# Kernel tuning notes

Hardware: AMD Instinct MI355X
Metric: run time of the kernel (lower is better)

## Reference

```python
import jax, jax.numpy as jnp
import numpy as np

NU, NI = 100000, 50000          # sampled users / items in the block
E = 1600000                      # edges (user-item interactions)
D = 64                           # hidden_dims
R = 6                            # num_ratings + 1


def setup_inputs() -> dict:
    key = jax.random.key(0)
    ks = jax.random.split(key, 24)
    f = jax.random.normal
    inp = {
        'user_ids': jax.random.randint(ks[0], (NU,), 0, 500000),
        'item_ids': jax.random.randint(ks[1], (NI,), 0, 200000),
        'gender': jax.random.randint(ks[2], (NU,), 0, 3),
        'genres': jax.random.randint(ks[3], (NI,), 0, 20),
        'edge_user': jax.random.randint(ks[4], (E,), 0, NU),
        'edge_item': jax.random.randint(ks[5], (E,), 0, NI),
        'rating': jax.random.randint(ks[6], (E,), 0, R),
        'user_emb': f(ks[7], (500000, D), jnp.float32),
        'item_emb': f(ks[8], (200000, D), jnp.float32),
        'gender_emb': f(ks[9], (3, D), jnp.float32),
        'genre_emb': f(ks[10], (20, D), jnp.float32),
        'Wr_watched': f(ks[11], (R, D, D), jnp.float32) * 0.1,
        'Wr_watchedby': f(ks[12], (R, D, D), jnp.float32) * 0.1,
        'Ww': f(ks[13], (D, 2 * D), jnp.float32) * 0.1,
        'bw': f(ks[14], (D,), jnp.float32) * 0.1,
        'Wwb': f(ks[15], (D, 2 * D), jnp.float32) * 0.1,
        'bwb': f(ks[16], (D,), jnp.float32) * 0.1,
        'Wf': f(ks[17], (D, D), jnp.float32) * 0.1,
        'bf': f(ks[18], (D,), jnp.float32) * 0.1,
        'Vf': f(ks[19], (D, D), jnp.float32) * 0.1,
        'bv': f(ks[20], (D,), jnp.float32) * 0.1,
    }
    return inp


def _gcmc_conv(Wr, Wlin, blin, h_src, h_dst, src_idx, dst_idx, rating, n_dst):
    # per-node relation transform: [R, N_src, D] (grouped GEMM instead of per-edge [E,D,D])
    X = jnp.einsum('nj,rij->rni', h_src, Wr)
    m = X[rating, src_idx]                              # per-edge message [E, D]
    s = jax.ops.segment_sum(m, dst_idx, num_segments=n_dst)
    cnt = jax.ops.segment_sum(jnp.ones((m.shape[0], 1), m.dtype), dst_idx,
                              num_segments=n_dst)
    h_neigh = s / jnp.maximum(cnt, 1.0)                 # mean; 0 for isolated nodes
    return jax.nn.relu(jnp.concatenate([h_dst, h_neigh], axis=1) @ Wlin.T + blin)


def reference(user_ids, item_ids, gender, genres, edge_user, edge_item, rating,
              user_emb, item_emb, gender_emb, genre_emb,
              Wr_watched, Wr_watchedby, Ww, bw, Wwb, bwb, Wf, bf, Vf, bv):
    hu = user_emb[user_ids] + gender_emb[gender]        # [NU, D]
    hi = item_emb[item_ids] + genre_emb[genres]         # [NI, D]
    # GCMCLayer: 'watched' (user -> item) and 'watchedby' (item -> user)
    hi_new = _gcmc_conv(Wr_watched, Ww, bw, hu, hi, edge_user, edge_item,
                        rating, hi.shape[0])
    hu_new = _gcmc_conv(Wr_watchedby, Wwb, bwb, hi, hu, edge_item, edge_user,
                        rating, hu.shape[0])
    user_out = hu_new @ Wf.T + bf
    item_out = hi_new @ Vf.T + bv
    return user_out, item_out
```

## Files before the change

kernel.cpp:

```cpp
#include <hip/hip_runtime.h>
#include <hip/hip_bf16.h>

#define D 64
#define NRAT 6

typedef float f32x4 __attribute__((ext_vector_type(4)));
typedef short bf16x8 __attribute__((ext_vector_type(8)));

union FragU { uint32_t u[4]; bf16x8 v; };

__device__ __forceinline__ short f2bf(float f) {
    __hip_bfloat16 h = __float2bfloat16(f);
    union { __hip_bfloat16 h; short s; } c; c.h = h; return c.s;
}
__device__ __forceinline__ uint32_t pk2(float a, float b) {
    union { short s[2]; uint32_t u; } c; c.s[0] = f2bf(a); c.s[1] = f2bf(b); return c.u;
}

__global__ void build_h(const int* __restrict__ uid, const int* __restrict__ iid,
                        const int* __restrict__ gender, const int* __restrict__ genres,
                        const float* __restrict__ user_emb, const float* __restrict__ item_emb,
                        const float* __restrict__ gender_emb, const float* __restrict__ genre_emb,
                        unsigned short* __restrict__ hu, unsigned short* __restrict__ hi,
                        int* __restrict__ cntZero, int NU, int NI) {
    int t = blockIdx.x * blockDim.x + threadIdx.x;
    if (t < 512) cntZero[t] = 0;
    int total = (NU + NI) * 16;
    if (t >= total) return;
    int row = t >> 4, c = t & 15;
    uint2 o;
    if (row < NU) {
        int u = uid[row], g = gender[row];
        float4 a = ((const float4*)user_emb)[(size_t)u * 16 + c];
        float4 b = ((const float4*)gender_emb)[(size_t)g * 16 + c];
        o.x = pk2(a.x + b.x, a.y + b.y); o.y = pk2(a.z + b.z, a.w + b.w);
        ((uint2*)hu)[(size_t)row * 16 + c] = o;
    } else {
        int r2 = row - NU;
        int it = iid[r2], ge = genres[r2];
        float4 a = ((const float4*)item_emb)[(size_t)it * 16 + c];
        float4 b = ((const float4*)genre_emb)[(size_t)ge * 16 + c];
        o.x = pk2(a.x + b.x, a.y + b.y); o.y = pk2(a.z + b.z, a.w + b.w);
        ((uint2*)hi)[(size_t)r2 * 16 + c] = o;
    }
}

__global__ __launch_bounds__(256) void hist_both(const int* __restrict__ edge_item,
                                                 const int* __restrict__ edge_user,
                                                 int* __restrict__ cntI, int* __restrict__ cntU,
                                                 int E) {
    __shared__ int hI[256], hU[256];
    hI[threadIdx.x] = 0; hU[threadIdx.x] = 0;
    __syncthreads();
    for (int i = blockIdx.x * blockDim.x + threadIdx.x; i < E; i += gridDim.x * blockDim.x) {
        atomicAdd(&hI[edge_item[i] >> 8], 1);
        atomicAdd(&hU[edge_user[i] >> 9], 1);
    }
    __syncthreads();
    int vi = hI[threadIdx.x], vu = hU[threadIdx.x];
    if (vi) atomicAdd(&cntI[threadIdx.x], vi);
    if (vu) atomicAdd(&cntU[threadIdx.x], vu);
}

__global__ __launch_bounds__(256) void scan_both(const int* __restrict__ cntI,
                                                 const int* __restrict__ cntU,
                                                 int* __restrict__ offI, int* __restrict__ offU,
                                                 int* __restrict__ curI, int* __restrict__ curU,
                                                 int NBI, int NBU, int E) {
    const int* cnt = blockIdx.x ? cntU : cntI;
    int* coarseOff  = blockIdx.x ? offU : offI;
    int* coarseCur  = blockIdx.x ? curU : curI;
    int NB          = blockIdx.x ? NBU : NBI;
    __shared__ int p[256];
    int tid = threadIdx.x;
    int v = (tid < NB) ? cnt[tid] : 0;
    p[tid] = v; __syncthreads();
    for (int dd = 1; dd < 256; dd <<= 1) {
        int a = (tid >= dd) ? p[tid - dd] : 0;
        __syncthreads();
        p[tid] += a;
        __syncthreads();
    }
    int excl = p[tid] - v;
    if (tid < NB) { coarseOff[tid] = excl; coarseCur[tid] = excl; }
    if (tid == 0) coarseOff[NB] = E;
}

__global__ __launch_bounds__(256) void multisplit_A2(
        const int* __restrict__ edge_item, const int* __restrict__ edge_user,
        const int* __restrict__ rating,
        int* __restrict__ curI, int* __restrict__ curU,
        unsigned* __restrict__ staged1, unsigned* __restrict__ staged2,
        int E, int nTiles, int NU, int NI) {
    const bool dirU = blockIdx.x >= nTiles;
    const int* dst = dirU ? edge_user : edge_item;
    const int* src = dirU ? edge_item : edge_user;
    const int shift = dirU ? 9 : 8;
    const int Ns = dirU ? NI : NU;
    int* coarseCur = dirU ? curU : curI;
    unsigned* staged = dirU ? staged2 : staged1;
    const int tile = (dirU ? blockIdx.x - nTiles : blockIdx.x) * 2048;

    __shared__ unsigned srt[2048];
    __shared__ int sft[2048];
    __shared__ int hist[256], pfx[256], shm[256];
    const int tid = threadIdx.x;
    int cnt = E - tile; if (cnt > 2048) cnt = 2048;
    hist[tid] = 0;
    __syncthreads();
    unsigned rec[8]; int bk[8];
    #pragma unroll
    for (int k = 0; k < 8; ++k) {
        int i = tile + k * 256 + tid;
        bk[k] = -1;
        if (i < E) {
            int d = dst[i], s = src[i], r = rating[i];
            bk[k] = d >> shift;
            rec[k] = (unsigned)(s + r * Ns) | ((unsigned)(d & ((1 << shift) - 1)) << 20);
            atomicAdd(&hist[bk[k]], 1);
        }
    }
    __syncthreads();
    pfx[tid] = hist[tid];
    __syncthreads();
    for (int dd = 1; dd < 256; dd <<= 1) {
        int a = (tid >= dd) ? pfx[tid - dd] : 0;
        __syncthreads();
        pfx[tid] += a;
        __syncthreads();
    }
    int h = hist[tid];
    int excl = pfx[tid] - h;
    int gb = 0;
    if (h > 0) gb = atomicAdd(&coarseCur[tid], h);
    shm[tid] = gb - excl;
    __syncthreads();
    hist[tid] = excl;
    __syncthreads();
    #pragma unroll
    for (int k = 0; k < 8; ++k) {
        if (bk[k] >= 0) {
            int p = atomicAdd(&hist[bk[k]], 1);
            srt[p] = rec[k];
            sft[p] = shm[bk[k]];
        }
    }
    __syncthreads();
    for (int i = tid; i < cnt; i += 256)
        staged[sft[i] + i] = srt[i];
}

__global__ __launch_bounds__(256) void multisplit_B2(
        unsigned* __restrict__ staged1, unsigned* __restrict__ staged2,
        const int* __restrict__ coarseOffI, const int* __restrict__ coarseOffU,
        int* __restrict__ offI, int* __restrict__ offU,
        int NBI, int NU, int NI, int E) {
    const bool dirU = (int)blockIdx.x >= NBI;
    unsigned* staged = dirU ? staged2 : staged1;
    const int* coarseOff = dirU ? coarseOffU : coarseOffI;
    int* off = dirU ? offU : offI;
    const int N = dirU ? NU : NI;
    const int shift = dirU ? 9 : 8;
    const int b = dirU ? blockIdx.x - NBI : blockIdx.x;
    const int nb = dirU ? (N + (1 << 9) - 1) >> 9 : NBI;

    __shared__ unsigned rec[16384];
    __shared__ int hist[512], pfx[512];
    const int tid = threadIdx.x;
    const int range = 1 << shift;
    int cbase = coarseOff[b];
    int cnt = coarseOff[b + 1] - cbase;
    if (cnt > 16384) cnt = 16384;
    hist[tid] = 0; hist[tid + 256] = 0;
    __syncthreads();
    for (int i = tid; i < cnt; i += 256) {
        unsigned x = staged[cbase + i];
        rec[i] = x;
        atomicAdd(&hist[x >> 20], 1);
    }
    __syncthreads();
    pfx[tid] = hist[tid]; pfx[tid + 256] = hist[tid + 256];
    __syncthreads();
    for (int dd = 1; dd < 256; dd <<= 1) {
        int a = (tid >= dd) ? pfx[tid - dd] : 0;
        int c = (tid >= dd) ? pfx[tid + 256 - dd] : 0;
        __syncthreads();
        pfx[tid] += a; pfx[tid + 256] += c;
        __syncthreads();
    }
    int tot0 = pfx[255];
    __syncthreads();
    pfx[tid + 256] += tot0;
    __syncthreads();
    int e0 = pfx[tid] - hist[tid];
    int e1 = pfx[tid + 256] - hist[tid + 256];
    __syncthreads();
    hist[tid] = e0; hist[tid + 256] = e1;
    int dbase = b << shift;
    if (dbase + tid < N) off[dbase + tid] = cbase + e0;
    if (range > 256 && dbase + tid + 256 < N) off[dbase + tid + 256] = cbase + e1;
    if (b == nb - 1 && tid == 0) off[N] = E;
    __syncthreads();
    for (int i = tid; i < cnt; i += 256) {
        unsigned x = rec[i];
        int p = atomicAdd(&hist[x >> 20], 1);
        staged[cbase + p] = x;
    }
}

__global__ void prep_weights(const float* __restrict__ Wr_w, const float* __restrict__ Wr_wb,
                             const float* __restrict__ Ww, const float* __restrict__ Wwb,
                             const float* __restrict__ Vf, const float* __restrict__ Wf,
                             short* __restrict__ pWrW, short* __restrict__ pWrWB,
                             short* __restrict__ pWw, short* __restrict__ pWwb,
                             short* __restrict__ pVf, short* __restrict__ pWf) {
    int t = blockIdx.x * blockDim.x + threadIdx.x;
    const float* src; short* dst; int K; int idx;
    if      (t < 24576) { src = Wr_w;  dst = pWrW;  K = 64;  idx = t; }
    else if (t < 49152) { src = Wr_wb; dst = pWrWB; K = 64;  idx = t - 24576; }
    else if (t < 57344) { src = Ww;    dst = pWw;   K = 128; idx = t - 49152; }
    else if (t < 65536) { src = Wwb;   dst = pWwb;  K = 128; idx = t - 57344; }
    else if (t < 69632) { src = Vf;    dst = pVf;   K = 64;  idx = t - 65536; }
    else if (t < 73728) { src = Wf;    dst = pWf;   K = 64;  idx = t - 69632; }
    else return;
    int per  = 64 * K;
    int sub  = idx / per;
    int li   = idx % per;
    int e    = li & 7;
    int lane = (li >> 3) & 63;
    int frag = li >> 9;
    int nkt  = K >> 5;
    int t16  = frag / nkt, tk = frag % nkt;
    int row  = t16 * 16 + (lane & 15);
    int col  = tk * 32 + (lane >> 4) * 8 + e;
    dst[idx] = f2bf(src[((size_t)(sub * 64 + row)) * K + col]);
}

__global__ __launch_bounds__(256) void pretransform2(
        const unsigned short* __restrict__ hu, const unsigned short* __restrict__ hi,
        const short* __restrict__ pWrW, const short* __restrict__ pWrWB,
        unsigned short* __restrict__ y1, unsigned short* __restrict__ y2,
        int NU, int NI, int wavesU) {
    const int lane = threadIdx.x & 63;
    const int m = lane & 15, q = lane >> 4;
    int wave = (blockIdx.x * blockDim.x + threadIdx.x) >> 6;
    const bool dirI = wave >= wavesU;
    const unsigned short* h = dirI ? hi : hu;
    const short* pWr = dirI ? pWrWB : pWrW;
    unsigned short* y = dirI ? y2 : y1;
    const int Ns = dirI ? NI : NU;
    if (dirI) wave -= wavesU;
    const int n0 = wave * 16;
    if (n0 >= Ns) return;
    int nrow = n0 + m; if (nrow > Ns - 1) nrow = Ns - 1;

    bf16x8 bB[2];
    {
        const unsigned short* ph = h + (size_t)nrow * D + q * 8;
        bB[0] = *(const bf16x8*)(ph);
        bB[1] = *(const bf16x8*)(ph + 32);
    }
    const int srcA = ((q & 1) << 5) + m;
    const int srcB = srcA + 16;
    const bool hiq = (q >> 1) != 0;

    #pragma unroll
    for (int r = 0; r < NRAT; ++r) {
        f32x4 acc[4] = {};
        #pragma unroll
        for (int it = 0; it < 4; ++it)
            #pragma unroll
            for (int kt = 0; kt < 2; ++kt) {
                bf16x8 a = *(const bf16x8*)(pWr + (((r * 4 + it) * 2 + kt) << 9) + (lane << 3));
                acc[it] = __builtin_amdgcn_mfma_f32_16x16x32_bf16(a, bB[kt], acc[it], 0, 0, 0);
            }
        uint32_t u0[4], u1[4];
        #pragma unroll
        for (int it = 0; it < 4; ++it) {
            u0[it] = pk2(acc[it][0], acc[it][1]);
            u1[it] = pk2(acc[it][2], acc[it][3]);
        }
        #pragma unroll
        for (int w = 0; w < 2; ++w) {
            uint32_t aa0 = (uint32_t)__shfl((int)u0[2*w],   srcA), bb0 = (uint32_t)__shfl((int)u0[2*w+1], srcA);
            uint32_t aa1 = (uint32_t)__shfl((int)u1[2*w],   srcA), bb1 = (uint32_t)__shfl((int)u1[2*w+1], srcA);
            uint32_t aa2 = (uint32_t)__shfl((int)u0[2*w],   srcB), bb2 = (uint32_t)__shfl((int)u0[2*w+1], srcB);
            uint32_t aa3 = (uint32_t)__shfl((int)u1[2*w],   srcB), bb3 = (uint32_t)__shfl((int)u1[2*w+1], srcB);
            FragU f;
            f.u[0] = hiq ? bb0 : aa0;
            f.u[1] = hiq ? bb1 : aa1;
            f.u[2] = hiq ? bb2 : aa2;
            f.u[3] = hiq ? bb3 : aa3;
            *(bf16x8*)(y + ((size_t)r * Ns + nrow) * D + w * 32 + q * 8) = f.v;
        }
    }
}

__global__ __launch_bounds__(256) void gather_both(
        const int* __restrict__ offI, const int* __restrict__ offU,
        const unsigned* __restrict__ staged1, const unsigned* __restrict__ staged2,
        const unsigned short* __restrict__ y1, const unsigned short* __restrict__ y2,
        unsigned short* __restrict__ hn1, unsigned short* __restrict__ hn2,
        int NI, int NU) {
    int lane = threadIdx.x & 63;
    int g = (blockIdx.x * blockDim.x + threadIdx.x) >> 6;
    const bool dirU = g >= NI;
    int n = dirU ? g - NI : g;
    if (dirU && n >= NU) return;
    const int* off = dirU ? offU : offI;
    const unsigned* packed = dirU ? staged2 : staged1;
    const unsigned short* y = dirU ? y2 : y1;
    unsigned short* hn = dirU ? hn2 : hn1;

    int b = off[n], e = off[n + 1];
    float a0 = 0.f, a1 = 0.f, a2 = 0.f, a3 = 0.f;

#define YLD(mm) __uint_as_float(((unsigned)y[((size_t)((mm) & 0xFFFFFu)) * D + lane]) << 16)

    for (int base = b; base < e; base += 64) {
        int idx = base + lane; if (idx > e - 1) idx = e - 1;
        unsigned meta = packed[idx];
        int cnt = e - base; if (cnt > 64) cnt = 64;
        int j = 0;
        for (; j + 4 <= cnt; j += 4) {
            unsigned m0 = (unsigned)__builtin_amdgcn_readlane((int)meta, j);
            unsigned m1 = (unsigned)__builtin_amdgcn_readlane((int)meta, j + 1);
            unsigned m2 = (unsigned)__builtin_amdgcn_readlane((int)meta, j + 2);
            unsigned m3 = (unsigned)__builtin_amdgcn_readlane((int)meta, j + 3);
            a0 += YLD(m0); a1 += YLD(m1); a2 += YLD(m2); a3 += YLD(m3);
        }
        for (; j < cnt; ++j) {
            unsigned mm = (unsigned)__builtin_amdgcn_readlane((int)meta, j);
            a0 += YLD(mm);
        }
    }
#undef YLD
    float inv = 1.0f / fmaxf((float)(e - b), 1.0f);
    hn[(size_t)n * D + lane] = (unsigned short)f2bf(((a0 + a1) + (a2 + a3)) * inv);
}

__global__ __launch_bounds__(256) void transform_both(
        const unsigned short* __restrict__ hn1, const unsigned short* __restrict__ hn2,
        const unsigned short* __restrict__ hi, const unsigned short* __restrict__ hu,
        const short* __restrict__ pWw, const short* __restrict__ pWwb,
        const float* __restrict__ bw, const float* __restrict__ bwb,
        const short* __restrict__ pVf, const short* __restrict__ pWf,
        const float* __restrict__ bv, const float* __restrict__ bf,
        float* __restrict__ item_out, float* __restrict__ user_out,
        int NI, int NU, int tilesI) {
    const int lane = threadIdx.x & 63;
    const int m = lane & 15, q = lane >> 4;
    int wave = (blockIdx.x * blockDim.x + threadIdx.x) >> 6;
    const bool dirU = wave >= tilesI;
    if (dirU) wave -= tilesI;
    const unsigned short* hn = dirU ? hn2 : hn1;
    const unsigned short* hd = dirU ? hu : hi;
    const short* pWlin = dirU ? pWwb : pWw;
    const float* blin  = dirU ? bwb : bw;
    const short* pW2   = dirU ? pWf : pVf;
    const float* b2    = dirU ? bf : bv;
    float* out = dirU ? user_out : item_out;
    const int N = dirU ? NU : NI;
    const int n0 = wave * 16;
    if (n0 >= N) return;
    int nrow = n0 + m; if (nrow > N - 1) nrow = N - 1;

    bf16x8 bH[2], bHN[2];
    {
        const unsigned short* ph = hd + (size_t)nrow * D + q * 8;
        bH[0] = *(const bf16x8*)(ph);
        bH[1] = *(const bf16x8*)(ph + 32);
        const unsigned short* pn = hn + (size_t)nrow * D + q * 8;
        bHN[0] = *(const bf16x8*)(pn);
        bHN[1] = *(const bf16x8*)(pn + 32);
    }

    f32x4 acc2[4] = {};
    #pragma unroll
    for (int it = 0; it < 4; ++it)
        #pragma unroll
        for (int kt = 0; kt < 4; ++kt) {
            bf16x8 a = *(const bf16x8*)(pWlin + (((it * 4) + kt) << 9) + (lane << 3));
            bf16x8 b = (kt < 2) ? bH[kt] : bHN[kt - 2];
            acc2[it] = __builtin_amdgcn_mfma_f32_16x16x32_bf16(a, b, acc2[it], 0, 0, 0);
        }

    const int srcA = ((q & 1) << 5) + m;
    const int srcB = srcA + 16;
    const bool hiq = (q >> 1) != 0;
    uint32_t u0[4], u1[4];
    float vbl = blin[lane];
    #pragma unroll
    for (int it = 0; it < 4; ++it) {
        float h0 = fmaxf(acc2[it][0] + __shfl(vbl, it * 16 + q * 4 + 0), 0.f);
        float h1 = fmaxf(acc2[it][1] + __shfl(vbl, it * 16 + q * 4 + 1), 0.f);
        float h2 = fmaxf(acc2[it][2] + __shfl(vbl, it * 16 + q * 4 + 2), 0.f);
        float h3 = fmaxf(acc2[it][3] + __shfl(vbl, it * 16 + q * 4 + 3), 0.f);
        u0[it] = pk2(h0, h1);
        u1[it] = pk2(h2, h3);
    }
    bf16x8 bA3[2];
    #pragma unroll
    for (int w = 0; w < 2; ++w) {
        uint32_t aa0 = (uint32_t)__shfl((int)u0[2*w],   srcA), bb0 = (uint32_t)__shfl((int)u0[2*w+1], srcA);
        uint32_t aa1 = (uint32_t)__shfl((int)u1[2*w],   srcA), bb1 = (uint32_t)__shfl((int)u1[2*w+1], srcA);
        uint32_t aa2 = (uint32_t)__shfl((int)u0[2*w],   srcB), bb2 = (uint32_t)__shfl((int)u0[2*w+1], srcB);
        uint32_t aa3 = (uint32_t)__shfl((int)u1[2*w],   srcB), bb3 = (uint32_t)__shfl((int)u1[2*w+1], srcB);
        FragU f;
        f.u[0] = hiq ? bb0 : aa0;
        f.u[1] = hiq ? bb1 : aa1;
        f.u[2] = hiq ? bb2 : aa2;
        f.u[3] = hiq ? bb3 : aa3;
        bA3[w] = f.v;
    }

    f32x4 acc3[4] = {};
    #pragma unroll
    for (int ct = 0; ct < 4; ++ct)
        #pragma unroll
        for (int kt = 0; kt < 2; ++kt) {
            bf16x8 b = *(const bf16x8*)(pW2 + (((ct * 2) + kt) << 9) + (lane << 3));
            acc3[ct] = __builtin_amdgcn_mfma_f32_16x16x32_bf16(bA3[kt], b, acc3[ct], 0, 0, 0);
        }
    #pragma unroll
    for (int ct = 0; ct < 4; ++ct) {
        float bb = b2[ct * 16 + m];
        #pragma unroll
        for (int rg = 0; rg < 4; ++rg) {
            int n = n0 + q * 4 + rg;
            if (n < N) out[(size_t)n * D + ct * 16 + m] = acc3[ct][rg] + bb;
        }
    }
}

extern "C" void kernel_launch(void* const* d_in, const int* in_sizes, int n_in,
                              void* d_out, int out_size, void* d_ws, size_t ws_size,
                              hipStream_t stream) {
    const int*   user_ids   = (const int*)  d_in[0];
    const int*   item_ids   = (const int*)  d_in[1];
    const int*   gender     = (const int*)  d_in[2];
    const int*   genres     = (const int*)  d_in[3];
    const int*   edge_user  = (const int*)  d_in[4];
    const int*   edge_item  = (const int*)  d_in[5];
    const int*   rating     = (const int*)  d_in[6];
    const float* user_emb   = (const float*)d_in[7];
    const float* item_emb   = (const float*)d_in[8];
    const float* gender_emb = (const float*)d_in[9];
    const float* genre_emb  = (const float*)d_in[10];
    const float* Wr_watched   = (const float*)d_in[11];
    const float* Wr_watchedby = (const float*)d_in[12];
    const float* Ww  = (const float*)d_in[13];
    const float* bw  = (const float*)d_in[14];
    const float* Wwb = (const float*)d_in[15];
    const float* bwb = (const float*)d_in[16];
    const float* Wf  = (const float*)d_in[17];
    const float* bf  = (const float*)d_in[18];
    const float* Vf  = (const float*)d_in[19];
    const float* bv  = (const float*)d_in[20];

    const int NU = in_sizes[0];
    const int NI = in_sizes[1];
    const int E  = in_sizes[4];
    const int NBI = (NI + 255) >> 8;
    const int NBU = (NU + 511) >> 9;

    float* out_f    = (float*)d_out;
    float* user_out = out_f;
    float* item_out = out_f + (size_t)NU * D;

    unsigned short* hu  = (unsigned short*)d_ws;
    unsigned short* hi  = hu  + (size_t)NU * D;
    unsigned short* hn1 = hi  + (size_t)NI * D;
    unsigned short* hn2 = hn1 + (size_t)NI * D;
    unsigned short* y1  = hn2 + (size_t)NU * D;
    unsigned short* y2  = y1  + (size_t)NRAT * NU * D;
    size_t bfElems = (size_t)(2 * NU + 2 * NI) * D + (size_t)NRAT * (NU + NI) * D;
    size_t byteOff = (bfElems * 2 + 15) & ~(size_t)15;
    short* pWrW  = (short*)((char*)d_ws + byteOff);
    short* pWrWB = pWrW  + 24576;
    short* pWw   = pWrWB + 24576;
    short* pWwb  = pWw   + 8192;
    short* pVf   = pWwb  + 8192;
    short* pWf   = pVf   + 4096;
    int* coarseCntI = (int*)(pWf + 4096);
    int* coarseCntU = coarseCntI + 256;
    int* coarseOffI = coarseCntU + 256;
    int* coarseOffU = coarseOffI + 257;
    int* coarseCurI = coarseOffU + 257;
    int* coarseCurU = coarseCurI + 256;
    int* offI   = coarseCurU + 256;
    int* offU   = offI + NI + 1;
    unsigned* staged1 = (unsigned*)(offU + NU + 1);
    unsigned* staged2 = staged1 + E;

    int totalh = (NU + NI) * 16;
    build_h<<<(totalh + 255) / 256, 256, 0, stream>>>(
        user_ids, item_ids, gender, genres,
        user_emb, item_emb, gender_emb, genre_emb, hu, hi, coarseCntI, NU, NI);
    prep_weights<<<288, 256, 0, stream>>>(Wr_watched, Wr_watchedby, Ww, Wwb, Vf, Wf,
                                          pWrW, pWrWB, pWw, pWwb, pVf, pWf);
    hist_both<<<512, 256, 0, stream>>>(edge_item, edge_user, coarseCntI, coarseCntU, E);
    scan_both<<<2, 256, 0, stream>>>(coarseCntI, coarseCntU, coarseOffI, coarseOffU,
                                     coarseCurI, coarseCurU, NBI, NBU, E);

    const int nTilesA = (E + 2047) / 2048;
    multisplit_A2<<<2 * nTilesA, 256, 0, stream>>>(edge_item, edge_user, rating,
                                                   coarseCurI, coarseCurU,
                                                   staged1, staged2, E, nTilesA, NU, NI);
    multisplit_B2<<<NBI + NBU, 256, 0, stream>>>(staged1, staged2, coarseOffI, coarseOffU,
                                                 offI, offU, NBI, NU, NI, E);

    {
        int wavesU = (NU + 15) / 16, wavesI = (NI + 15) / 16;
        int blocks = (wavesU + wavesI + 3) / 4;
        pretransform2<<<blocks, 256, 0, stream>>>(hu, hi, pWrW, pWrWB, y1, y2, NU, NI, wavesU);
    }
    gather_both<<<(NI + NU + 3) / 4, 256, 0, stream>>>(offI, offU, staged1, staged2,
                                                       y1, y2, hn1, hn2, NI, NU);
    {
        int tilesI = (NI + 15) / 16, tilesU = (NU + 15) / 16;
        int blocks = (tilesI + tilesU + 3) / 4;
        transform_both<<<blocks, 256, 0, stream>>>(hn1, hn2, hi, hu, pWw, pWwb, bw, bwb,
                                                   pVf, pWf, bv, bf, item_out, user_out,
                                                   NI, NU, tilesI);
    }
}
```

Baseline: 244.7 us.

## Gather two bf16 per lane with half-wave edge split; merge weight prep into build kernel

The gather kernel now loads 32-bit pairs of bf16 values. Each half-wave handles a different edge, so one wave processes two edges per load, and the two halves are combined with a cross-lane shuffle at the end. This is meant to cut the number of memory instructions and raise the effective width of each load in the dominant gather phase. Separately, the weight-packing kernel is folded into the embedding-build kernel, which removes one launch. The cost is extra shuffles and a more complex tail path, and the fused build kernel relies on having at least 74752 threads in its grid.

```diff
diff --git a/kernel.cpp b/kernel.cpp
--- a/kernel.cpp
+++ b/kernel.cpp
@@ -17,14 +17,44 @@
     union { short s[2]; uint32_t u; } c; c.s[0] = f2bf(a); c.s[1] = f2bf(b); return c.u;
 }
 
-__global__ void build_h(const int* __restrict__ uid, const int* __restrict__ iid,
-                        const int* __restrict__ gender, const int* __restrict__ genres,
-                        const float* __restrict__ user_emb, const float* __restrict__ item_emb,
-                        const float* __restrict__ gender_emb, const float* __restrict__ genre_emb,
-                        unsigned short* __restrict__ hu, unsigned short* __restrict__ hi,
-                        int* __restrict__ cntZero, int NU, int NI) {
+__global__ void build_setup(const int* __restrict__ uid, const int* __restrict__ iid,
+                            const int* __restrict__ gender, const int* __restrict__ genres,
+                            const float* __restrict__ user_emb, const float* __restrict__ item_emb,
+                            const float* __restrict__ gender_emb, const float* __restrict__ genre_emb,
+                            unsigned short* __restrict__ hu, unsigned short* __restrict__ hi,
+                            int* __restrict__ zeroRegion,
+                            const float* __restrict__ Wr_w, const float* __restrict__ Wr_wb,
+                            const float* __restrict__ Ww, const float* __restrict__ Wwb,
+                            const float* __restrict__ Vf, const float* __restrict__ Wf,
+                            short* __restrict__ pWrW, short* __restrict__ pWrWB,
+                            short* __restrict__ pWw, short* __restrict__ pWwb,
+                            short* __restrict__ pVf, short* __restrict__ pWf,
+                            int NU, int NI) {
     int t = blockIdx.x * blockDim.x + threadIdx.x;
-    if (t < 512) cntZero[t] = 0;
+    if (t < 512) zeroRegion[t] = 0;
+
+    int tp = t - 1024;
+    if (tp >= 0 && tp < 73728) {
+        const float* src; short* dst; int K; int idx;
+        if      (tp < 24576) { src = Wr_w;  dst = pWrW;  K = 64;  idx = tp; }
+        else if (tp < 49152) { src = Wr_wb; dst = pWrWB; K = 64;  idx = tp - 24576; }
+        else if (tp < 57344) { src = Ww;    dst = pWw;   K = 128; idx = tp - 49152; }
+        else if (tp < 65536) { src = Wwb;   dst = pWwb;  K = 128; idx = tp - 57344; }
+        else if (tp < 69632) { src = Vf;    dst = pVf;   K = 64;  idx = tp - 65536; }
+        else                 { src = Wf;    dst = pWf;   K = 64;  idx = tp - 69632; }
+        int per  = 64 * K;
+        int sub  = idx / per;
+        int li   = idx % per;
+        int e    = li & 7;
+        int lane = (li >> 3) & 63;
+        int frag = li >> 9;
+        int nkt  = K >> 5;
+        int t16  = frag / nkt, tk = frag % nkt;
+        int row  = t16 * 16 + (lane & 15);
+        int col  = tk * 32 + (lane >> 4) * 8 + e;
+        dst[idx] = f2bf(src[((size_t)(sub * 64 + row)) * K + col]);
+    }
+
     int total = (NU + NI) * 16;
     if (t >= total) return;
     int row = t >> 4, c = t & 15;
@@ -208,34 +238,6 @@
     }
 }
 
-__global__ void prep_weights(const float* __restrict__ Wr_w, const float* __restrict__ Wr_wb,
-                             const float* __restrict__ Ww, const float* __restrict__ Wwb,
-                             const float* __restrict__ Vf, const float* __restrict__ Wf,
-                             short* __restrict__ pWrW, short* __restrict__ pWrWB,
-                             short* __restrict__ pWw, short* __restrict__ pWwb,
-                             short* __restrict__ pVf, short* __restrict__ pWf) {
-    int t = blockIdx.x * blockDim.x + threadIdx.x;
-    const float* src; short* dst; int K; int idx;
-    if      (t < 24576) { src = Wr_w;  dst = pWrW;  K = 64;  idx = t; }
-    else if (t < 49152) { src = Wr_wb; dst = pWrWB; K = 64;  idx = t - 24576; }
-    else if (t < 57344) { src = Ww;    dst = pWw;   K = 128; idx = t - 49152; }
-    else if (t < 65536) { src = Wwb;   dst = pWwb;  K = 128; idx = t - 57344; }
-    else if (t < 69632) { src = Vf;    dst = pVf;   K = 64;  idx = t - 65536; }
-    else if (t < 73728) { src = Wf;    dst = pWf;   K = 64;  idx = t - 69632; }
-    else return;
-    int per  = 64 * K;
-    int sub  = idx / per;
-    int li   = idx % per;
-    int e    = li & 7;
-    int lane = (li >> 3) & 63;
-    int frag = li >> 9;
-    int nkt  = K >> 5;
-    int t16  = frag / nkt, tk = frag % nkt;
-    int row  = t16 * 16 + (lane & 15);
-    int col  = tk * 32 + (lane >> 4) * 8 + e;
-    dst[idx] = f2bf(src[((size_t)(sub * 64 + row)) * K + col]);
-}
-
 __global__ __launch_bounds__(256) void pretransform2(
         const unsigned short* __restrict__ hu, const unsigned short* __restrict__ hi,
         const short* __restrict__ pWrW, const short* __restrict__ pWrWB,
@@ -299,23 +301,27 @@
 __global__ __launch_bounds__(256) void gather_both(
         const int* __restrict__ offI, const int* __restrict__ offU,
         const unsigned* __restrict__ staged1, const unsigned* __restrict__ staged2,
-        const unsigned short* __restrict__ y1, const unsigned short* __restrict__ y2,
-        unsigned short* __restrict__ hn1, unsigned short* __restrict__ hn2,
+        const unsigned* __restrict__ y1, const unsigned* __restrict__ y2,
+        unsigned* __restrict__ hn1, unsigned* __restrict__ hn2,
         int NI, int NU) {
-    int lane = threadIdx.x & 63;
+    const int lane = threadIdx.x & 63;
+    const int half = lane >> 5;
+    const int l5   = lane & 31;
     int g = (blockIdx.x * blockDim.x + threadIdx.x) >> 6;
     const bool dirU = g >= NI;
     int n = dirU ? g - NI : g;
     if (dirU && n >= NU) return;
     const int* off = dirU ? offU : offI;
     const unsigned* packed = dirU ? staged2 : staged1;
-    const unsigned short* y = dirU ? y2 : y1;
-    unsigned short* hn = dirU ? hn2 : hn1;
+    const unsigned* y = dirU ? y2 : y1;
+    unsigned* hn = dirU ? hn2 : hn1;
 
     int b = off[n], e = off[n + 1];
-    float a0 = 0.f, a1 = 0.f, a2 = 0.f, a3 = 0.f;
-
-#define YLD(mm) __uint_as_float(((unsigned)y[((size_t)((mm) & 0xFFFFFu)) * D + lane]) << 16)
+    float a0 = 0.f, a1 = 0.f;
+
+#define YPAIR(mm) y[(((mm) << 5) & 0x1FFFFE0u) | (unsigned)l5]
+#define ACC2(dd) { a0 += __uint_as_float((dd) << 16); \
+                   a1 += __uint_as_float((dd) & 0xFFFF0000u); }
 
     for (int base = b; base < e; base += 64) {
         int idx = base + lane; if (idx > e - 1) idx = e - 1;
@@ -323,20 +329,32 @@
         int cnt = e - base; if (cnt > 64) cnt = 64;
         int j = 0;
         for (; j + 4 <= cnt; j += 4) {
-            unsigned m0 = (unsigned)__builtin_amdgcn_readlane((int)meta, j);
-            unsigned m1 = (unsigned)__builtin_amdgcn_readlane((int)meta, j + 1);
-            unsigned m2 = (unsigned)__builtin_amdgcn_readlane((int)meta, j + 2);
-            unsigned m3 = (unsigned)__builtin_amdgcn_readlane((int)meta, j + 3);
-            a0 += YLD(m0); a1 += YLD(m1); a2 += YLD(m2); a3 += YLD(m3);
-        }
-        for (; j < cnt; ++j) {
+            unsigned mA = (unsigned)__shfl((int)meta, j + half);
+            unsigned mB = (unsigned)__shfl((int)meta, j + 2 + half);
+            unsigned dA = YPAIR(mA);
+            unsigned dB = YPAIR(mB);
+            ACC2(dA); ACC2(dB);
+        }
+        if (j + 2 <= cnt) {
+            unsigned mA = (unsigned)__shfl((int)meta, j + half);
+            unsigned dA = YPAIR(mA);
+            ACC2(dA);
+            j += 2;
+        }
+        if (j < cnt) {
             unsigned mm = (unsigned)__builtin_amdgcn_readlane((int)meta, j);
-            a0 += YLD(mm);
-        }
-    }
-#undef YLD
+            if (half == 0) { unsigned dd = YPAIR(mm); ACC2(dd); }
+        }
+    }
+#undef YPAIR
+#undef ACC2
+
+    float o0 = __shfl(a0, lane ^ 32);
+    float o1 = __shfl(a1, lane ^ 32);
     float inv = 1.0f / fmaxf((float)(e - b), 1.0f);
-    hn[(size_t)n * D + lane] = (unsigned short)f2bf(((a0 + a1) + (a2 + a3)) * inv);
+    float s0 = (a0 + o0) * inv;
+    float s1 = (a1 + o1) * inv;
+    if (lane < 32) hn[(size_t)n * 32 + l5] = pk2(s0, s1);
 }
 
 __global__ __launch_bounds__(256) void transform_both(
@@ -494,11 +512,12 @@
     unsigned* staged2 = staged1 + E;
 
     int totalh = (NU + NI) * 16;
-    build_h<<<(totalh + 255) / 256, 256, 0, stream>>>(
+    build_setup<<<(totalh + 255) / 256, 256, 0, stream>>>(
         user_ids, item_ids, gender, genres,
-        user_emb, item_emb, gender_emb, genre_emb, hu, hi, coarseCntI, NU, NI);
-    prep_weights<<<288, 256, 0, stream>>>(Wr_watched, Wr_watchedby, Ww, Wwb, Vf, Wf,
-                                          pWrW, pWrWB, pWw, pWwb, pVf, pWf);
+        user_emb, item_emb, gender_emb, genre_emb, hu, hi, coarseCntI,
+        Wr_watched, Wr_watchedby, Ww, Wwb, Vf, Wf,
+        pWrW, pWrWB, pWw, pWwb, pVf, pWf, NU, NI);
+
     hist_both<<<512, 256, 0, stream>>>(edge_item, edge_user, coarseCntI, coarseCntU, E);
     scan_both<<<2, 256, 0, stream>>>(coarseCntI, coarseCntU, coarseOffI, coarseOffU,
                                      coarseCurI, coarseCurU, NBI, NBU, E);
@@ -516,7 +535,8 @@
         pretransform2<<<blocks, 256, 0, stream>>>(hu, hi, pWrW, pWrWB, y1, y2, NU, NI, wavesU);
     }
     gather_both<<<(NI + NU + 3) / 4, 256, 0, stream>>>(offI, offU, staged1, staged2,
-                                                       y1, y2, hn1, hn2, NI, NU);
+                                                       (const unsigned*)y1, (const unsigned*)y2,
+                                                       (unsigned*)hn1, (unsigned*)hn2, NI, NU);
     {
         int tilesI = (NI + 15) / 16, tilesU = (NU + 15) / 16;
         int blocks = (tilesI + tilesU + 3) / 4;
```

New measurement: 236.6 us. -3.3%, faster.
